# Optimization experiments

Hardware: AMD Instinct MI355X
Metric: run time of the kernel (lower is better)

Reference implementation:

```python
import jax, jax.numpy as jnp
import numpy as np

B, S, D, H = 4, 1024, 512, 8
HD = D // H          # head_dim = 64
WIN = 32
EMB_HID = 128
NEG = -1e10


def _rel_coords_log():
    # __make_pair_wise_relative_positions: 2D meshgrid over window indexes
    idx = jnp.arange(WIN)
    coords = jnp.stack(jnp.meshgrid(idx, idx, indexing='ij'), 0).reshape(2, -1)  # [2, S]
    rel = coords[:, :, None] - coords[:, None, :]                                # [2, S, S]
    rel = rel.transpose(1, 2, 0).reshape(-1, 2).astype(jnp.float32)              # [S*S, 2]
    return jnp.sign(rel) * jnp.log1p(jnp.abs(rel))


def setup_inputs() -> dict:
    key = jax.random.key(0)
    ks = jax.random.split(key, 16)
    sd = 1.0 / np.sqrt(D)
    p = lambda k, sh, s: (jax.random.normal(k, sh, jnp.float32) * s)
    return {
        'query': jax.random.normal(ks[0], (B, S, D), jnp.float32),
        'key':   jax.random.normal(ks[1], (B, S, D), jnp.float32),
        'value': jax.random.normal(ks[2], (B, S, D), jnp.float32),
        'mask':  jnp.ones((B, 1, 1, S), jnp.int64),
        'Wq': p(ks[3], (D, D), sd), 'bq': jnp.zeros((D,), jnp.float32),
        'Wk': p(ks[4], (D, D), sd), 'bk': jnp.zeros((D,), jnp.float32),
        'Wv': p(ks[5], (D, D), sd), 'bv': jnp.zeros((D,), jnp.float32),
        'Wo': p(ks[6], (D, D), sd), 'bo': jnp.zeros((D,), jnp.float32),
        'W1': p(ks[7], (2, EMB_HID), 0.7), 'b1': jnp.zeros((EMB_HID,), jnp.float32),
        'W2': p(ks[8], (EMB_HID, H), 0.1), 'b2': jnp.zeros((H,), jnp.float32),
    }


def reference(query, key, value, mask, Wq, bq, Wk, bk, Wv, bv, Wo, bo, W1, b1, W2, b2):
    scale = jnp.sqrt(jnp.float32(HD))
    Q = (query @ Wq + bq).reshape(B, S, H, HD).transpose(0, 2, 1, 3)  # [B,H,S,HD]
    K = (key   @ Wk + bk).reshape(B, S, H, HD).transpose(0, 2, 1, 3)
    V = (value @ Wv + bv).reshape(B, S, H, HD).transpose(0, 2, 1, 3)

    energy = jnp.einsum('bhqd,bhkd->bhqk', Q, K) / scale             # [B,H,S,S]

    # continuous position bias: MLP(2 -> EMB_HID -> H) on log-spaced rel coords
    rel = _rel_coords_log()                                           # [S*S, 2]
    bias = jax.nn.relu(rel @ W1 + b1) @ W2 + b2                       # [S*S, H]
    bias = bias.T.reshape(H, S, S)[None]                              # [1,H,S,S]
    energy = energy + bias

    energy = jnp.where(mask == 0, NEG, energy)
    attention = jax.nn.softmax(energy, axis=-1)                       # [B,H,S,S]
    x = jnp.einsum('bhqk,bhkd->bhqd', attention, V)                   # dropout p=0
    x = x.transpose(0, 2, 1, 3).reshape(B, S, D)
    x = x @ Wo + bo
    return x, attention
```

## Files before the change

kernel.cpp:

```cpp
#include <hip/hip_runtime.h>
#include <hip/hip_bf16.h>

typedef __attribute__((ext_vector_type(4))) float f32x4;
typedef __attribute__((ext_vector_type(8))) short bf16x8;
typedef __attribute__((ext_vector_type(4))) unsigned short u16x4;

#define DEVI __device__ __forceinline__

constexpr int B_ = 4, S_ = 1024, D_ = 512, H_ = 8, HD_ = 64;
constexpr float CSH = 11.0903548f;

DEVI unsigned short f2b(float f) {
  union { float f; unsigned u; } v; v.f = f;
  unsigned r = v.u + 0x7fffu + ((v.u >> 16) & 1u);
  return (unsigned short)(r >> 16);
}

DEVI float b2f(unsigned short u) {
  union { unsigned u; float f; } v; v.u = ((unsigned)u) << 16;
  return v.f;
}

__global__ __launch_bounds__(256) void k_prep(const float* Wa, const float* Wb,
                                              const float* Wc, const float* Wd,
                                              unsigned short* T0, unsigned short* T1,
                                              unsigned short* T2, unsigned short* T3,
                                              const float* mW1, const float* mb1,
                                              const float* mW2, const float* mb2,
                                              float* table) {
  if (blockIdx.z == 4) {
    if (blockIdx.y != 0) return;
    int idx = blockIdx.x * 256 + threadIdx.x;
    if (idx >= 63 * 63) return;
    int dy = idx / 63 - 31, dx = idx % 63 - 31;
    float r0 = copysignf(log1pf(fabsf((float)dy)), (float)dy);
    float r1 = copysignf(log1pf(fabsf((float)dx)), (float)dx);
    float acc[8];
#pragma unroll
    for (int h = 0; h < 8; ++h) acc[h] = mb2[h];
    for (int j = 0; j < 128; ++j) {
      float hv = fmaxf(r0 * mW1[j] + r1 * mW1[128 + j] + mb1[j], 0.f);
#pragma unroll
      for (int h = 0; h < 8; ++h) acc[h] += hv * mW2[j * 8 + h];
    }
#pragma unroll
    for (int h = 0; h < 8; ++h) table[h * 3969 + idx] = acc[h] - CSH;
    return;
  }
  const float* W = blockIdx.z == 0 ? Wa : blockIdx.z == 1 ? Wb : blockIdx.z == 2 ? Wc : Wd;
  unsigned short* T = blockIdx.z == 0 ? T0 : blockIdx.z == 1 ? T1 : blockIdx.z == 2 ? T2 : T3;
  __shared__ float tile[32][33];
  int tx = threadIdx.x & 31, ty = threadIdx.x >> 5;
  int n0 = blockIdx.x * 32, k0 = blockIdx.y * 32;
#pragma unroll
  for (int r = 0; r < 4; ++r) tile[ty + r * 8][tx] = W[(size_t)(k0 + ty + r * 8) * D_ + n0 + tx];
  __syncthreads();
#pragma unroll
  for (int r = 0; r < 4; ++r) T[(size_t)(n0 + ty + r * 8) * D_ + k0 + tx] = f2b(tile[tx][ty + r * 8]);
}

__global__ __launch_bounds__(256) void k_gemm_qkv(const float* Aq, const float* Ak, const float* Av,
                                                  const unsigned short* Tq, const unsigned short* Tk,
                                                  const unsigned short* Tv,
                                                  const float* bqv, const float* bkv, const float* bvv,
                                                  unsigned short* Oq, unsigned short* Ok,
                                                  unsigned short* OvT) {
  const float* A = blockIdx.z == 0 ? Aq : blockIdx.z == 1 ? Ak : Av;
  const unsigned short* BT = blockIdx.z == 0 ? Tq : blockIdx.z == 1 ? Tk : Tv;
  const float* bias = blockIdx.z == 0 ? bqv : blockIdx.z == 1 ? bkv : bvv;

  __shared__ unsigned short As[64][72];
  __shared__ unsigned short Bs[128][72];
  const int tid = threadIdx.x;
  const int lane = tid & 63, wave = tid >> 6;
  const int lr = lane & 15, lg = lane >> 4;
  const int wm = (wave >> 1) * 32, wn = (wave & 1) * 64;
  const int m0 = blockIdx.x * 64, n0 = blockIdx.y * 128;

  f32x4 acc[2][4];
#pragma unroll
  for (int i = 0; i < 2; ++i)
#pragma unroll
    for (int j = 0; j < 4; ++j) acc[i][j] = (f32x4){0.f, 0.f, 0.f, 0.f};

  for (int k0 = 0; k0 < 512; k0 += 64) {
#pragma unroll
    for (int i = 0; i < 4; ++i) {
      int idx = tid + i * 256;
      int r = idx >> 4, c4 = (idx & 15) * 4;
      float4 fv = *(const float4*)(A + (size_t)(m0 + r) * 512 + k0 + c4);
      u16x4 wv;
      wv[0] = f2b(fv.x); wv[1] = f2b(fv.y); wv[2] = f2b(fv.z); wv[3] = f2b(fv.w);
      *(u16x4*)&As[r][c4] = wv;
    }
#pragma unroll
    for (int i = 0; i < 8; ++i) {
      int idx = tid + i * 256;
      int r = idx >> 4, c4 = (idx & 15) * 4;
      *(u16x4*)&Bs[r][c4] = *(const u16x4*)(BT + (size_t)(n0 + r) * 512 + k0 + c4);
    }
    __syncthreads();
#pragma unroll
    for (int kk = 0; kk < 2; ++kk) {
      bf16x8 af[2], bg[4];
#pragma unroll
      for (int i = 0; i < 2; ++i) af[i] = *(const bf16x8*)&As[wm + i * 16 + lr][kk * 32 + lg * 8];
#pragma unroll
      for (int j = 0; j < 4; ++j) bg[j] = *(const bf16x8*)&Bs[wn + j * 16 + lr][kk * 32 + lg * 8];
#pragma unroll
      for (int i = 0; i < 2; ++i)
#pragma unroll
        for (int j = 0; j < 4; ++j)
          acc[i][j] = __builtin_amdgcn_mfma_f32_16x16x32_bf16(af[i], bg[j], acc[i][j], 0, 0, 0);
    }
    __syncthreads();
  }

#pragma unroll
  for (int i = 0; i < 2; ++i)
#pragma unroll
    for (int j = 0; j < 4; ++j) {
      int mbase = m0 + wm + i * 16 + lg * 4;
      int n = n0 + wn + j * 16 + lr;
      float bvl = bias[n];
      int h = n >> 6, hd = n & 63;
      int bseg = mbase >> 10, s0 = mbase & 1023;
      if (blockIdx.z == 2) {
        u16x4 pk;
#pragma unroll
        for (int r = 0; r < 4; ++r) pk[r] = f2b(acc[i][j][r] + bvl);
        *(u16x4*)(OvT + (((size_t)(bseg * H_ + h) * 64 + hd) * 1024 + s0)) = pk;
      } else {
        unsigned short* outp = blockIdx.z == 0 ? Oq : Ok;
#pragma unroll
        for (int r = 0; r < 4; ++r) {
          float v = acc[i][j][r] + bvl;
          outp[(((size_t)bseg * H_ + h) * S_ + s0 + r) * HD_ + hd] = f2b(v);
        }
      }
    }
}

__global__ __launch_bounds__(256) void k_gemm_out(const unsigned short* A, const unsigned short* BT,
                                                  const float* bias, float* outp) {
  __shared__ unsigned short As[64][72];
  __shared__ unsigned short Bs[128][72];
  const int tid = threadIdx.x;
  const int lane = tid & 63, wave = tid >> 6;
  const int lr = lane & 15, lg = lane >> 4;
  const int wm = (wave >> 1) * 32, wn = (wave & 1) * 64;
  const int m0 = blockIdx.x * 64, n0 = blockIdx.y * 128;

  f32x4 acc[2][4];
#pragma unroll
  for (int i = 0; i < 2; ++i)
#pragma unroll
    for (int j = 0; j < 4; ++j) acc[i][j] = (f32x4){0.f, 0.f, 0.f, 0.f};

  for (int k0 = 0; k0 < 512; k0 += 64) {
#pragma unroll
    for (int i = 0; i < 4; ++i) {
      int idx = tid + i * 256;
      int r = idx >> 4, c4 = (idx & 15) * 4;
      *(u16x4*)&As[r][c4] = *(const u16x4*)(A + (size_t)(m0 + r) * 512 + k0 + c4);
    }
#pragma unroll
    for (int i = 0; i < 8; ++i) {
      int idx = tid + i * 256;
      int r = idx >> 4, c4 = (idx & 15) * 4;
      *(u16x4*)&Bs[r][c4] = *(const u16x4*)(BT + (size_t)(n0 + r) * 512 + k0 + c4);
    }
    __syncthreads();
#pragma unroll
    for (int kk = 0; kk < 2; ++kk) {
      bf16x8 af[2], bg[4];
#pragma unroll
      for (int i = 0; i < 2; ++i) af[i] = *(const bf16x8*)&As[wm + i * 16 + lr][kk * 32 + lg * 8];
#pragma unroll
      for (int j = 0; j < 4; ++j) bg[j] = *(const bf16x8*)&Bs[wn + j * 16 + lr][kk * 32 + lg * 8];
#pragma unroll
      for (int i = 0; i < 2; ++i)
#pragma unroll
        for (int j = 0; j < 4; ++j)
          acc[i][j] = __builtin_amdgcn_mfma_f32_16x16x32_bf16(af[i], bg[j], acc[i][j], 0, 0, 0);
    }
    __syncthreads();
  }

#pragma unroll
  for (int i = 0; i < 2; ++i)
#pragma unroll
    for (int j = 0; j < 4; ++j) {
      int mbase = m0 + wm + i * 16 + lg * 4;
      int n = n0 + wn + j * 16 + lr;
      float bvl = bias[n];
#pragma unroll
      for (int r = 0; r < 4; ++r)
        outp[(size_t)(mbase + r) * 512 + n] = acc[i][j][r] + bvl;
    }
}

__global__ __launch_bounds__(256, 2) void k_attn(const unsigned short* Qb, const unsigned short* Kb,
                                                 const unsigned short* VT, const float* tbl,
                                                 const int* mask, float* out_attn,
                                                 unsigned short* Xp) {
  const int tid = threadIdx.x;
  const int lane = tid & 63, w = tid >> 6;
  const int lr = lane & 15, lg = lane >> 4;
  const int bh = blockIdx.y, b = bh >> 3, h = bh & 7;
  const int q0 = blockIdx.x * 16;

  __shared__ unsigned short Pb[16][1024];
  __shared__ unsigned short KV[4][64][64];
  __shared__ float biasS[2016];
  __shared__ float mbig[1024];
  __shared__ float lsbuf[4][16];
  __shared__ int tbad[16];

  const unsigned short* Qh = Qb + (size_t)bh * (S_ * HD_);
  const unsigned short* Kh = Kb + (size_t)bh * (S_ * HD_);
  const unsigned short* Vth = VT + (size_t)bh * (HD_ * S_);

  if (tid < 16) tbad[tid] = 0;
  __syncthreads();
  {
    const float* tsl = tbl + h * 3969 + (q0 >> 5) * 63;
    for (int i = tid; i < 2016; i += 256) biasS[i] = tsl[i];
  }
  {
    int4 mv = *(const int4*)(mask + b * S_ + tid * 4);
    int base = tid * 4;
    mbig[base] = mv.x ? 3.0e38f : -30.f;
    mbig[base + 1] = mv.y ? 3.0e38f : -30.f;
    mbig[base + 2] = mv.z ? 3.0e38f : -30.f;
    mbig[base + 3] = mv.w ? 3.0e38f : -30.f;
    if (!(mv.x && mv.y && mv.z && mv.w)) tbad[base >> 6] = 1;
  }

  const int qrow = q0 + lr;
  const bf16x8 bq0 = *(const bf16x8*)(Qh + (size_t)qrow * 64 + lg * 8);
  const bf16x8 bq1 = *(const bf16x8*)(Qh + (size_t)qrow * 64 + 32 + lg * 8);
  const int qj31 = (q0 & 31) + lr + 31;

  float ls = 0.f;
  __syncthreads();

  const int srow8 = lane >> 3, sch = lane & 7;
  bf16x8 kpre[8];
#pragma unroll
  for (int i = 0; i < 8; ++i) {
    int row = i * 8 + srow8;
    kpre[i] = *(const bf16x8*)(Kh + (size_t)((w * 4) * 64 + row) * 64 + sch * 8);
  }
#pragma unroll
  for (int it = 0; it < 4; ++it) {
    const int gt = w * 4 + it;
#pragma unroll
    for (int i = 0; i < 8; ++i) {
      int row = i * 8 + srow8;
      *(bf16x8*)&KV[w][row][(sch ^ (row & 7)) * 8] = kpre[i];
    }
    if (it < 3) {
#pragma unroll
      for (int i = 0; i < 8; ++i) {
        int row = i * 8 + srow8;
        kpre[i] = *(const bf16x8*)(Kh + (size_t)((gt + 1) * 64 + row) * 64 + sch * 8);
      }
    }
    const bool bad = tbad[gt] != 0;
#pragma unroll
    for (int fn = 0; fn < 4; ++fn) {
      const unsigned short* krow = &KV[w][fn * 16 + lr][0];
      bf16x8 a0 = *(const bf16x8*)(krow + (lg ^ (lr & 7)) * 8);
      bf16x8 a1 = *(const bf16x8*)(krow + ((4 + lg) ^ (lr & 7)) * 8);
      f32x4 s = (f32x4){0.f, 0.f, 0.f, 0.f};
      s = __builtin_amdgcn_mfma_f32_16x16x32_bf16(a0, bq0, s, 0, 0, 0);
      s = __builtin_amdgcn_mfma_f32_16x16x32_bf16(a1, bq1, s, 0, 0, 0);
      u16x4 pb;
#pragma unroll
      for (int r = 0; r < 4; ++r) {
        int bidx = (31 - gt * 2 - (fn >> 1)) * 63 + qj31 - (fn & 1) * 16 - lg * 4 - r;
        float arg = fmaf(s[r], 0.125f, biasS[bidx]);
        if (bad) arg = fminf(arg, mbig[gt * 64 + fn * 16 + lg * 4 + r]);
        float p = __expf(arg);
        ls += p;
        pb[r] = f2b(p);
      }
      int s8 = (gt * 16 + fn * 4 + lg) ^ ((lr & 7) << 1);
      *(u16x4*)((char*)&Pb[lr][0] + s8 * 8) = pb;
    }
  }
  ls += __shfl_xor(ls, 16, 64);
  ls += __shfl_xor(ls, 32, 64);
  if (lg == 0) lsbuf[w][lr] = ls;
  __syncthreads();

  const float inv = 1.f / (lsbuf[0][lr] + lsbuf[1][lr] + lsbuf[2][lr] + lsbuf[3][lr]);

  f32x4 invs;
#pragma unroll
  for (int j = 0; j < 4; ++j) invs[j] = __shfl(inv, j * 4 + lg, 64);
  float* oa = out_attn + (size_t)bh * (S_ * S_) + (size_t)q0 * S_ + w * 256;
#pragma unroll
  for (int i = 0; i < 16; ++i) {
    int qv = (i & 3) * 4 + lg;
    int kk = (i >> 2) * 64 + lr * 4;
    int s8 = ((w * 256 + kk) >> 2) ^ ((qv & 7) << 1);
    u16x4 pb = *(const u16x4*)((const char*)&Pb[qv][0] + s8 * 8);
    f32x4 pr;
#pragma unroll
    for (int r = 0; r < 4; ++r) pr[r] = b2f(pb[r]) * invs[i & 3];
    *(f32x4*)(oa + (size_t)qv * S_ + kk) = pr;
  }

  f32x4 of = (f32x4){0.f, 0.f, 0.f, 0.f};
  bf16x8 vp0 = *(const bf16x8*)(Vth + (size_t)(w * 16 + (lane >> 3)) * S_ + (lane & 7) * 8);
  bf16x8 vp1 = *(const bf16x8*)(Vth + (size_t)(w * 16 + 8 + (lane >> 3)) * S_ + (lane & 7) * 8);
#pragma unroll
  for (int gt = 0; gt < 16; ++gt) {
    {
      int row0 = lane >> 3, ch = lane & 7;
      *(bf16x8*)&KV[w][row0][(ch ^ (row0 & 7)) * 8] = vp0;
      int row1 = 8 + (lane >> 3);
      *(bf16x8*)&KV[w][row1][(ch ^ (row1 & 7)) * 8] = vp1;
    }
    if (gt < 15) {
      vp0 = *(const bf16x8*)(Vth + (size_t)(w * 16 + (lane >> 3)) * S_ + (gt + 1) * 64 + (lane & 7) * 8);
      vp1 = *(const bf16x8*)(Vth + (size_t)(w * 16 + 8 + (lane >> 3)) * S_ + (gt + 1) * 64 + (lane & 7) * 8);
    }
#pragma unroll
    for (int sub = 0; sub < 2; ++sub) {
      int c16 = (gt * 8 + sub * 4 + lg) ^ (lr & 7);
      bf16x8 pa = *(const bf16x8*)((const char*)&Pb[lr][0] + c16 * 16);
      bf16x8 bv = *(const bf16x8*)((const char*)&KV[w][lr][0] + ((sub * 4 + lg) ^ (lr & 7)) * 16);
      of = __builtin_amdgcn_mfma_f32_16x16x32_bf16(pa, bv, of, 0, 0, 0);
    }
  }

  f32x4 invq;
#pragma unroll
  for (int r = 0; r < 4; ++r) invq[r] = __shfl(inv, lg * 4 + r, 64);
#pragma unroll
  for (int r = 0; r < 4; ++r) {
    int q = q0 + lg * 4 + r;
    Xp[((size_t)b * S_ + q) * D_ + h * 64 + w * 16 + lr] = f2b(of[r] * invq[r]);
  }
}

extern "C" void kernel_launch(void* const* d_in, const int* in_sizes, int n_in,
                              void* d_out, int out_size, void* d_ws, size_t ws_size,
                              hipStream_t stream) {
  const float* query = (const float*)d_in[0];
  const float* key   = (const float*)d_in[1];
  const float* value = (const float*)d_in[2];
  const int*   maskp = (const int*)d_in[3];
  const float* Wq = (const float*)d_in[4];
  const float* bq = (const float*)d_in[5];
  const float* Wk = (const float*)d_in[6];
  const float* bk = (const float*)d_in[7];
  const float* Wv = (const float*)d_in[8];
  const float* bv = (const float*)d_in[9];
  const float* Wo = (const float*)d_in[10];
  const float* bo = (const float*)d_in[11];
  const float* W1 = (const float*)d_in[12];
  const float* b1 = (const float*)d_in[13];
  const float* W2 = (const float*)d_in[14];
  const float* b2 = (const float*)d_in[15];

  char* ws = (char*)d_ws;
  const size_t MB4 = (size_t)4 * 1024 * 1024;
  unsigned short* Qb  = (unsigned short*)(ws);
  unsigned short* Kb  = (unsigned short*)(ws + MB4);
  unsigned short* VT  = (unsigned short*)(ws + 2 * MB4);
  unsigned short* Xp  = (unsigned short*)(ws + 3 * MB4);
  unsigned short* WqT = (unsigned short*)(ws + 4 * MB4);
  unsigned short* WkT = (unsigned short*)(ws + 4 * MB4 + 524288);
  unsigned short* WvT = (unsigned short*)(ws + 4 * MB4 + 2 * 524288);
  unsigned short* WoT = (unsigned short*)(ws + 4 * MB4 + 3 * 524288);
  float* table        = (float*)(ws + 4 * MB4 + 4 * 524288);

  float* out_x = (float*)d_out;
  float* out_attn = out_x + (size_t)B_ * S_ * D_;

  k_prep<<<dim3(16, 16, 5), 256, 0, stream>>>(Wq, Wk, Wv, Wo, WqT, WkT, WvT, WoT,
                                              W1, b1, W2, b2, table);
  k_gemm_qkv<<<dim3(64, 4, 3), 256, 0, stream>>>(query, key, value, WqT, WkT, WvT,
                                                 bq, bk, bv, Qb, Kb, VT);
  k_attn<<<dim3(64, 32), 256, 0, stream>>>(Qb, Kb, VT, table, maskp, out_attn, Xp);
  k_gemm_out<<<dim3(64, 4), 256, 0, stream>>>(Xp, WoT, bo, out_x);
}
```

Before: 108.5 us.

## Load K and V fragments directly from global memory, dropping LDS staging

Removes the per-wave shared-memory staging buffer for K and V tiles. MFMA operand fragments are now read straight from global memory, which eliminates the LDS writes and reads plus the register prefetch arrays. The lower LDS footprint allows raising the launch-bounds occupancy hint from 2 to 3 blocks per CU. In exchange, it loses explicit software prefetching and relies on the cache for reuse, so global-load latency may be exposed more directly.

```diff
diff --git a/kernel.cpp b/kernel.cpp
--- a/kernel.cpp
+++ b/kernel.cpp
@@ -200,7 +200,7 @@
     }
 }
 
-__global__ __launch_bounds__(256, 2) void k_attn(const unsigned short* Qb, const unsigned short* Kb,
+__global__ __launch_bounds__(256, 3) void k_attn(const unsigned short* Qb, const unsigned short* Kb,
                                                  const unsigned short* VT, const float* tbl,
                                                  const int* mask, float* out_attn,
                                                  unsigned short* Xp) {
@@ -211,7 +211,6 @@
   const int q0 = blockIdx.x * 16;
 
   __shared__ unsigned short Pb[16][1024];
-  __shared__ unsigned short KV[4][64][64];
   __shared__ float biasS[2016];
   __shared__ float mbig[1024];
   __shared__ float lsbuf[4][16];
@@ -245,34 +244,15 @@
   float ls = 0.f;
   __syncthreads();
 
-  const int srow8 = lane >> 3, sch = lane & 7;
-  bf16x8 kpre[8];
-#pragma unroll
-  for (int i = 0; i < 8; ++i) {
-    int row = i * 8 + srow8;
-    kpre[i] = *(const bf16x8*)(Kh + (size_t)((w * 4) * 64 + row) * 64 + sch * 8);
-  }
 #pragma unroll
   for (int it = 0; it < 4; ++it) {
     const int gt = w * 4 + it;
-#pragma unroll
-    for (int i = 0; i < 8; ++i) {
-      int row = i * 8 + srow8;
-      *(bf16x8*)&KV[w][row][(sch ^ (row & 7)) * 8] = kpre[i];
-    }
-    if (it < 3) {
-#pragma unroll
-      for (int i = 0; i < 8; ++i) {
-        int row = i * 8 + srow8;
-        kpre[i] = *(const bf16x8*)(Kh + (size_t)((gt + 1) * 64 + row) * 64 + sch * 8);
-      }
-    }
     const bool bad = tbad[gt] != 0;
 #pragma unroll
     for (int fn = 0; fn < 4; ++fn) {
-      const unsigned short* krow = &KV[w][fn * 16 + lr][0];
-      bf16x8 a0 = *(const bf16x8*)(krow + (lg ^ (lr & 7)) * 8);
-      bf16x8 a1 = *(const bf16x8*)(krow + ((4 + lg) ^ (lr & 7)) * 8);
+      const unsigned short* kb = Kh + (size_t)(gt * 64 + fn * 16 + lr) * 64 + lg * 8;
+      bf16x8 a0 = *(const bf16x8*)(kb);
+      bf16x8 a1 = *(const bf16x8*)(kb + 32);
       f32x4 s = (f32x4){0.f, 0.f, 0.f, 0.f};
       s = __builtin_amdgcn_mfma_f32_16x16x32_bf16(a0, bq0, s, 0, 0, 0);
       s = __builtin_amdgcn_mfma_f32_16x16x32_bf16(a1, bq1, s, 0, 0, 0);
@@ -314,25 +294,14 @@
   }
 
   f32x4 of = (f32x4){0.f, 0.f, 0.f, 0.f};
-  bf16x8 vp0 = *(const bf16x8*)(Vth + (size_t)(w * 16 + (lane >> 3)) * S_ + (lane & 7) * 8);
-  bf16x8 vp1 = *(const bf16x8*)(Vth + (size_t)(w * 16 + 8 + (lane >> 3)) * S_ + (lane & 7) * 8);
+  const unsigned short* vb = Vth + (size_t)(w * 16 + lr) * 1024 + lg * 8;
 #pragma unroll
   for (int gt = 0; gt < 16; ++gt) {
-    {
-      int row0 = lane >> 3, ch = lane & 7;
-      *(bf16x8*)&KV[w][row0][(ch ^ (row0 & 7)) * 8] = vp0;
-      int row1 = 8 + (lane >> 3);
-      *(bf16x8*)&KV[w][row1][(ch ^ (row1 & 7)) * 8] = vp1;
-    }
-    if (gt < 15) {
-      vp0 = *(const bf16x8*)(Vth + (size_t)(w * 16 + (lane >> 3)) * S_ + (gt + 1) * 64 + (lane & 7) * 8);
-      vp1 = *(const bf16x8*)(Vth + (size_t)(w * 16 + 8 + (lane >> 3)) * S_ + (gt + 1) * 64 + (lane & 7) * 8);
-    }
 #pragma unroll
     for (int sub = 0; sub < 2; ++sub) {
       int c16 = (gt * 8 + sub * 4 + lg) ^ (lr & 7);
       bf16x8 pa = *(const bf16x8*)((const char*)&Pb[lr][0] + c16 * 16);
-      bf16x8 bv = *(const bf16x8*)((const char*)&KV[w][lr][0] + ((sub * 4 + lg) ^ (lr & 7)) * 16);
+      bf16x8 bv = *(const bf16x8*)(vb + gt * 64 + sub * 32);
       of = __builtin_amdgcn_mfma_f32_16x16x32_bf16(pa, bv, of, 0, 0, 0);
     }
   }
```

After: 120.9 us. +11.5%, slower.
